# Performance work log

Hardware: AMD Instinct MI355X
Metric: run time of the kernel (lower is better)

The kernel has to match this reference:

```python
import jax, jax.numpy as jnp
import numpy as np

NUM_HEADS = 16
HEAD_DIM = 64
HIDDEN = NUM_HEADS * HEAD_DIM  # 1024
B, S = 2, 2048
INV_NORM = 1.0 / np.sqrt(HEAD_DIM)


def setup_inputs() -> dict:
    key = jax.random.key(0)
    ks = jax.random.split(key, 8)
    hidden_states = jax.random.normal(ks[0], (1, B, S, HIDDEN), dtype=jnp.float32)
    residual = jax.random.normal(ks[1], (B, S, HIDDEN), dtype=jnp.float32)
    # ALiBi bias per (batch*head) broadcast over query positions: [B*H, 1, S]
    slopes = 2.0 ** (-8.0 * (jnp.arange(1, NUM_HEADS + 1, dtype=jnp.float32) / NUM_HEADS))
    pos = jnp.arange(S, dtype=jnp.float32)
    alibi = (slopes[:, None] * pos[None, :])[None]  # [1, H, S]
    alibi = jnp.broadcast_to(alibi, (B, NUM_HEADS, S)).reshape(B * NUM_HEADS, 1, S)
    # causal mask: True = masked out
    attention_mask = jnp.triu(jnp.ones((S, S), dtype=jnp.bool_), k=1)[None, None]  # [1,1,S,S]
    attention_mask = jnp.broadcast_to(attention_mask, (B, 1, S, S))
    W_qkv = jax.random.normal(ks[2], (3 * HIDDEN, HIDDEN), dtype=jnp.float32) * 0.02
    b_qkv = jax.random.normal(ks[3], (3 * HIDDEN,), dtype=jnp.float32) * 0.02
    W_dense = jax.random.normal(ks[4], (HIDDEN, HIDDEN), dtype=jnp.float32) * 0.02
    b_dense = jax.random.normal(ks[5], (HIDDEN,), dtype=jnp.float32) * 0.02
    return {
        "hidden_states": hidden_states,
        "residual": residual,
        "alibi": alibi,
        "attention_mask": attention_mask,
        "W_qkv": W_qkv,
        "b_qkv": b_qkv,
        "W_dense": W_dense,
        "b_dense": b_dense,
    }


def reference(hidden_states, residual, alibi, attention_mask, W_qkv, b_qkv, W_dense, b_dense):
    x = hidden_states[0]  # [B, S, H]
    b, s, _ = x.shape
    fused = x @ W_qkv.T + b_qkv  # [B, S, 3H]
    # Bloom interleaved split: [B, S, nh, 3, hd]
    qkv = fused.reshape(b, s, NUM_HEADS, 3, HEAD_DIM)
    q = jnp.transpose(qkv[..., 0, :], (0, 2, 1, 3))  # [B, nh, S, hd]
    k = jnp.transpose(qkv[..., 1, :], (0, 2, 1, 3))
    v = jnp.transpose(qkv[..., 2, :], (0, 2, 1, 3))
    # baddbmm: alibi + inv_norm * q @ k^T
    scores = jnp.einsum("bhqd,bhkd->bhqk", q, k) * INV_NORM
    scores = scores + alibi.reshape(b, NUM_HEADS, 1, s)  # [B, nh, S, S]
    neg_min = jnp.finfo(scores.dtype).min
    scores = jnp.where(attention_mask, neg_min, scores)
    probs = jax.nn.softmax(scores.astype(jnp.float32), axis=-1).astype(x.dtype)
    ctx = jnp.einsum("bhqk,bhkd->bhqd", probs, v)  # [B, nh, S, hd]
    ctx = jnp.transpose(ctx, (0, 2, 1, 3)).reshape(b, s, HIDDEN)  # merge_heads
    out = ctx @ W_dense.T + b_dense
    return out + residual  # dropout_add, eval mode
```

## Files before the change

### kernel.cpp

```cpp
#include <hip/hip_runtime.h>
#include <hip/hip_bf16.h>

#define NUM_HEADS 16
#define HEAD_DIM  64
#define HIDDEN    1024
#define BATCH     2
#define SEQ       2048
#define K_DIM     1024
#define INV_NORM  0.125f
#define LOG2E     1.4426950408889634f
#define IN2       (INV_NORM * LOG2E)

typedef __attribute__((ext_vector_type(4)))  float f32x4;
typedef __attribute__((ext_vector_type(16))) float f32x16;
typedef __attribute__((ext_vector_type(8)))  short bf16x8;
typedef __attribute__((ext_vector_type(4)))  unsigned int u32x4;
typedef __attribute__((ext_vector_type(2)))  unsigned int u32x2;
typedef unsigned short u16;

__device__ inline u16 f2bf(float f) {
    __hip_bfloat16 h = __float2bfloat16(f);
    return __builtin_bit_cast(u16, h);
}
__device__ inline float bf2f(u16 u) {
    unsigned int v = ((unsigned int)u) << 16;
    return __builtin_bit_cast(float, v);
}
__device__ inline float fexp2(float x) { return __builtin_exp2f(x); }

__device__ inline f32x16 mfma32(bf16x8 a, bf16x8 b, f32x16 c) {
    return __builtin_amdgcn_mfma_f32_32x32x16_bf16(a, b, c, 0, 0, 0);
}

__device__ inline void gl_lds16(const u16* g, u16* s) {
    __builtin_amdgcn_global_load_lds(
        (const __attribute__((address_space(1))) unsigned int*)g,
        (__attribute__((address_space(3))) unsigned int*)s, 16, 0, 0);
}

__global__ __launch_bounds__(256) void cvt_all(
        const float* __restrict__ x, const float* __restrict__ wq,
        const float* __restrict__ wd,
        u16* __restrict__ xb, u16* __restrict__ wqb, u16* __restrict__ wdb) {
    int i = (blockIdx.x * 256 + threadIdx.x) * 4;
    const float* s; u16* d; int off;
    if (i < 4194304)      { s = x;  d = xb;  off = i; }
    else if (i < 7340032) { s = wq; d = wqb; off = i - 4194304; }
    else                  { s = wd; d = wdb; off = i - 7340032; }
    const float4 v = *reinterpret_cast<const float4*>(s + off);
    ushort4 o;
    o.x = f2bf(v.x); o.y = f2bf(v.y); o.z = f2bf(v.z); o.w = f2bf(v.w);
    *reinterpret_cast<ushort4*>(d + off) = o;
}

#define GEMM_CORE(A_, B_)                                                              \
    const int tid = threadIdx.x;                                                       \
    const int w = tid >> 6, l = tid & 63;                                              \
    const int la = l & 31, hi = l >> 5;                                                \
    const int wr = w >> 1, wc = w & 1;                                                 \
    const int kperm = (((l & 7) ^ (l >> 3)) << 3);                                     \
    const u16* gA = A_ + (size_t)(mblk + w * 32 + (l >> 3)) * K_DIM + kperm;           \
    const u16* gB = B_ + (size_t)(nblk + w * 32 + (l >> 3)) * K_DIM + kperm;           \
    const int sca = (la & 7) << 3;                                                     \
    f32x16 acc[2][2] = {};                                                             \
    for (int kt = 0; kt < 16; ++kt) {                                                  \
        const int ko = kt * 64;                                                        \
        _Pragma("unroll")                                                              \
        for (int i = 0; i < 4; ++i) {                                                  \
            gl_lds16(gA + i * 8 * K_DIM + ko, &As[(w * 32 + i * 8) * 64]);             \
            gl_lds16(gB + i * 8 * K_DIM + ko, &Bs[(w * 32 + i * 8) * 64]);             \
        }                                                                              \
        asm volatile("s_waitcnt vmcnt(0)" ::: "memory");                               \
        __syncthreads();                                                               \
        const u16* pA = &As[(wr * 64 + la) * 64];                                      \
        const u16* pB = &Bs[(wc * 64 + la) * 64];                                      \
        _Pragma("unroll")                                                              \
        for (int kk = 0; kk < 4; ++kk) {                                               \
            const int co = (kk * 16 + hi * 8) ^ sca;                                   \
            bf16x8 a0 = *reinterpret_cast<const bf16x8*>(pA + co);                     \
            bf16x8 a1 = *reinterpret_cast<const bf16x8*>(pA + 32 * 64 + co);           \
            bf16x8 b0 = *reinterpret_cast<const bf16x8*>(pB + co);                     \
            bf16x8 b1 = *reinterpret_cast<const bf16x8*>(pB + 32 * 64 + co);           \
            acc[0][0] = mfma32(a0, b0, acc[0][0]);                                     \
            acc[0][1] = mfma32(a0, b1, acc[0][1]);                                     \
            acc[1][0] = mfma32(a1, b0, acc[1][0]);                                     \
            acc[1][1] = mfma32(a1, b1, acc[1][1]);                                     \
        }                                                                              \
        __syncthreads();                                                               \
    }

__global__ __launch_bounds__(256) void gemm_qkv(
        const u16* __restrict__ A, const u16* __restrict__ W,
        const float* __restrict__ bias,
        u16* __restrict__ qo, u16* __restrict__ ko2, u16* __restrict__ vTo) {
    __shared__ u16 As[128 * 64];
    __shared__ u16 Bs[128 * 64];
    int lin = blockIdx.x;
    int g = lin & 7, i2 = lin >> 3;
    const int mblk = ((g & 3) * 8 + (i2 & 7)) * 128;
    const int nblk = ((g >> 2) * 12 + (i2 >> 3)) * 128;
    GEMM_CORE(A, W)
    #pragma unroll
    for (int mi = 0; mi < 2; ++mi)
    #pragma unroll
    for (int ni = 0; ni < 2; ++ni) {
        int c = nblk + wc * 64 + ni * 32 + la;
        int h = c / 192, rem = c - h * 192;
        int which = rem >> 6, d = rem & 63;
        float bv = bias[c];
        #pragma unroll
        for (int r = 0; r < 16; ++r) {
            int m = mblk + wr * 64 + mi * 32 + (r & 3) + 8 * (r >> 2) + 4 * hi;
            int bb = m >> 11, s = m & (SEQ - 1);
            int bh = bb * NUM_HEADS + h;
            int t = s >> 5;
            size_t tb = ((size_t)(bh * 64 + t)) * 2048;
            u16 o = f2bf(acc[mi][ni][r] + bv);
            if (which == 2) {
                int dblk = d >> 5, ra = d & 31;
                int k = s & 31, ks = k >> 4, hf = (k >> 3) & 1, e = k & 7;
                vTo[tb + (dblk * 2 + ks) * 512 + hf * 256 + ra * 8 + e] = o;
            } else {
                int kk = d >> 4, hf = (d >> 3) & 1, e = d & 7, ra = s & 31;
                size_t off = tb + kk * 512 + hf * 256 + ra * 8 + e;
                if (which == 0) qo[off] = o;
                else            ko2[off] = o;
            }
        }
    }
}

__global__ __launch_bounds__(256) void gemm_dense(
        const u16* __restrict__ A, const u16* __restrict__ W,
        const float* __restrict__ bias, const float* __restrict__ residual,
        float* __restrict__ out) {
    __shared__ u16 As[128 * 64];
    __shared__ u16 Bs[128 * 64];
    int lin = blockIdx.x;
    int g = lin & 7, i2 = lin >> 3;
    const int mblk = ((g & 1) * 16 + (i2 & 15)) * 128;
    const int nblk = ((g >> 1) * 2 + (i2 >> 4)) * 128;
    GEMM_CORE(A, W)
    #pragma unroll
    for (int mi = 0; mi < 2; ++mi)
    #pragma unroll
    for (int ni = 0; ni < 2; ++ni) {
        int c = nblk + wc * 64 + ni * 32 + la;
        float bv = bias[c];
        #pragma unroll
        for (int r = 0; r < 16; ++r) {
            int m = mblk + wr * 64 + mi * 32 + (r & 3) + 8 * (r >> 2) + 4 * hi;
            out[(size_t)m * HIDDEN + c] = acc[mi][ni][r] + bv + residual[(size_t)m * HIDDEN + c];
        }
    }
}

__global__ __launch_bounds__(256) void knorm_max(const u16* __restrict__ Kf,
                                                 float* __restrict__ kn,
                                                 unsigned int* __restrict__ ctr) {
    if (blockIdx.x == 0 && threadIdx.x < 8) ctr[threadIdx.x] = 0;
    __shared__ float red[256];
    const int bh = blockIdx.x;
    float mx = 0.f;
    for (int s = threadIdx.x; s < SEQ; s += 256) {
        const u16* kp = Kf + ((size_t)(bh * 64 + (s >> 5))) * 2048 + (s & 31) * 8;
        float ss = 0.f;
        #pragma unroll
        for (int kk = 0; kk < 4; ++kk)
        #pragma unroll
        for (int hf = 0; hf < 2; ++hf) {
            bf16x8 v = *reinterpret_cast<const bf16x8*>(kp + kk * 512 + hf * 256);
            #pragma unroll
            for (int e = 0; e < 8; ++e) {
                float f = bf2f((u16)v[e]);
                ss = fmaf(f, f, ss);
            }
        }
        mx = fmaxf(mx, ss);
    }
    red[threadIdx.x] = mx;
    __syncthreads();
    for (int off = 128; off; off >>= 1) {
        if (threadIdx.x < (unsigned)off)
            red[threadIdx.x] = fmaxf(red[threadIdx.x], red[threadIdx.x + off]);
        __syncthreads();
    }
    if (threadIdx.x == 0) kn[bh] = sqrtf(red[0]);
}


#define LOADT(P, tt) {                                                        \
    const u16* kp_ = kbase + (size_t)(tt) * 2048;                             \
    P##k0 = *reinterpret_cast<const bf16x8*>(kp_);                            \
    P##k1 = *reinterpret_cast<const bf16x8*>(kp_ + 512);                      \
    P##k2 = *reinterpret_cast<const bf16x8*>(kp_ + 1024);                     \
    P##k3 = *reinterpret_cast<const bf16x8*>(kp_ + 1536);                     \
    const u16* vp_ = vbase + (size_t)(tt) * 2048;                             \
    P##v0 = *reinterpret_cast<const bf16x8*>(vp_);                            \
    P##v1 = *reinterpret_cast<const bf16x8*>(vp_ + 512);                      \
    P##v2 = *reinterpret_cast<const bf16x8*>(vp_ + 1024);                     \
    P##v3 = *reinterpret_cast<const bf16x8*>(vp_ + 1536);                     \
}

#define STEP(P, N, tcur, tnxt, DIAG) {                                        \
    f32x16 sca_ = {}, scb_ = {};                                              \
    sca_ = mfma32(P##k0, qf0, sca_);                                          \
    scb_ = mfma32(P##k1, qf1, scb_);                                          \
    sca_ = mfma32(P##k2, qf2, sca_);                                          \
    scb_ = mfma32(P##k3, qf3, scb_);                                          \
    LOADT(N, tnxt)                                                            \
    const float Dt_ = slope2 * (float)((tcur) * 32 - qw);                     \
    float p[16];                                                              \
    _Pragma("unroll")                                                         \
    for (int r = 0; r < 16; ++r)                                              \
        p[r] = __builtin_amdgcn_exp2f(fmaf(sca_[r] + scb_[r], IN2, cl[r] + Dt_)); \
    if (DIAG) {                                                               \
        _Pragma("unroll")                                                     \
        for (int r = 0; r < 16; ++r) {                                        \
            int kr_ = (r & 3) + 8 * (r >> 2) + 4 * hi;                        \
            if (kr_ > la) p[r] = 0.f;                                         \
        }                                                                     \
    }                                                                         \
    l_i += ((p[0] + p[1]) + (p[2] + p[3])) + ((p[4] + p[5]) + (p[6] + p[7]))  \
         + ((p[8] + p[9]) + (p[10] + p[11])) + ((p[12] + p[13]) + (p[14] + p[15])); \
    unsigned pk_[8];                                                          \
    _Pragma("unroll")                                                         \
    for (int m = 0; m < 4; ++m) {                                             \
        unsigned b0_ = __builtin_bit_cast(unsigned, p[4 * m])     + 0x8000u;  \
        unsigned b1_ = __builtin_bit_cast(unsigned, p[4 * m + 1]) + 0x8000u;  \
        unsigned b2_ = __builtin_bit_cast(unsigned, p[4 * m + 2]) + 0x8000u;  \
        unsigned b3_ = __builtin_bit_cast(unsigned, p[4 * m + 3]) + 0x8000u;  \
        pk_[2 * m]     = __builtin_amdgcn_perm(b1_, b0_, 0x07060302u);        \
        pk_[2 * m + 1] = __builtin_amdgcn_perm(b3_, b2_, 0x07060302u);        \
    }                                                                         \
    u32x2 r0_ = __builtin_amdgcn_permlane32_swap(pk_[0], pk_[2], false, false); \
    u32x2 r1_ = __builtin_amdgcn_permlane32_swap(pk_[1], pk_[3], false, false); \
    u32x2 r2_ = __builtin_amdgcn_permlane32_swap(pk_[4], pk_[6], false, false); \
    u32x2 r3_ = __builtin_amdgcn_permlane32_swap(pk_[5], pk_[7], false, false); \
    u32x4 pb0_, pb1_;                                                         \
    pb0_[0] = r0_[0]; pb0_[1] = r1_[0]; pb0_[2] = r0_[1]; pb0_[3] = r1_[1];   \
    pb1_[0] = r2_[0]; pb1_[1] = r3_[0]; pb1_[2] = r2_[1]; pb1_[3] = r3_[1];   \
    bf16x8 pf0_ = __builtin_bit_cast(bf16x8, pb0_);                           \
    bf16x8 pf1_ = __builtin_bit_cast(bf16x8, pb1_);                           \
    o0 = mfma32(P##v0, pf0_, o0);                                             \
    o0 = mfma32(P##v1, pf1_, o0);                                             \
    o1 = mfma32(P##v2, pf0_, o1);                                             \
    o1 = mfma32(P##v3, pf1_, o1);                                             \
}

__global__ __launch_bounds__(256) void attn(
        const u16* __restrict__ Qf, const u16* __restrict__ Kf,
        const u16* __restrict__ Vf, const float* __restrict__ alibi,
        const float* __restrict__ kn, u16* __restrict__ ctx,
        unsigned int* __restrict__ ctr) {
    __shared__ float o_l[4][64][33];
    __shared__ float ml[4][32];
    __shared__ unsigned int s_idx;
    const int grp  = blockIdx.x & 7;
    const int wave = __builtin_amdgcn_readfirstlane(threadIdx.x >> 6);
    const int lane = threadIdx.x & 63;
    const int la = lane & 31, hi = lane >> 5;

    for (;;) {
        if (threadIdx.x == 0) s_idx = atomicAdd(ctr + grp, 1u);
        __syncthreads();
        const unsigned int idx = s_idx;
        if (idx >= 256) return;
        int h, b, qt;
        if (idx < 128) { h = 15 - grp; qt = 63 - (int)(idx >> 1); b = idx & 1; }
        else           { h = grp; int j = idx - 128; qt = 63 - (j >> 1); b = j & 1; }
        const int bh = b * 16 + h;
        const int qw = qt * 32;
        const size_t tbh = (size_t)bh * 64;
        const float slope2 = alibi[(size_t)bh * SEQ + 1] * LOG2E;

        const u16* qp = Qf + (tbh + qt) * 2048 + lane * 8;
        bf16x8 qf0 = *reinterpret_cast<const bf16x8*>(qp);
        bf16x8 qf1 = *reinterpret_cast<const bf16x8*>(qp + 512);
        bf16x8 qf2 = *reinterpret_cast<const bf16x8*>(qp + 1024);
        bf16x8 qf3 = *reinterpret_cast<const bf16x8*>(qp + 1536);

        float qss = 0.f;
        #pragma unroll
        for (int e = 0; e < 8; ++e) {
            float f;
            f = bf2f((u16)qf0[e]); qss = fmaf(f, f, qss);
            f = bf2f((u16)qf1[e]); qss = fmaf(f, f, qss);
            f = bf2f((u16)qf2[e]); qss = fmaf(f, f, qss);
            f = bf2f((u16)qf3[e]); qss = fmaf(f, f, qss);
        }
        qss += __shfl_xor(qss, 32);
        float qmx = qss;
        #pragma unroll
        for (int off = 1; off <= 16; off <<= 1) qmx = fmaxf(qmx, __shfl_xor(qmx, off));
        const float kb = sqrtf(qmx) * kn[bh] * IN2;

        const float Wf = (47.f + 2.f * kb) / slope2;
        const int lo_k = qw - 31 - (int)Wf;
        const int t_lo = lo_k <= 0 ? 0 : ((lo_k + 31) >> 5);

        float cl[16];
        #pragma unroll
        for (int r = 0; r < 16; ++r)
            cl[r] = slope2 * (float)((r & 3) + 8 * (r >> 2) + 4 * hi - la) - kb;

        f32x16 o0 = {}, o1 = {};
        float l_i = 0.f;

        const int t0 = qt - wave;
        if (t0 >= t_lo) {
            const u16* kbase = Kf + tbh * 2048 + lane * 8;
            const u16* vbase = Vf + tbh * 2048 + lane * 8;
            const int nit = ((t0 - t_lo) >> 2) + 1;
            bf16x8 ak0, ak1, ak2, ak3, av0, av1, av2, av3;
            bf16x8 bk0, bk1, bk2, bk3, bv0, bv1, bv2, bv3;
            LOADT(a, t0)
            {
                const int tn1 = (nit > 1) ? t0 - 4 : t0;
                if (wave == 0) { STEP(a, b, t0, tn1, 1) }
                else           { STEP(a, b, t0, tn1, 0) }
            }
            int i = 1;
            while (i < nit) {
                {
                    const int tc = t0 - 4 * i;
                    const int tn = (i + 1 < nit) ? tc - 4 : tc;
                    STEP(b, a, tc, tn, 0)
                }
                ++i;
                if (i >= nit) break;
                {
                    const int tc = t0 - 4 * i;
                    const int tn = (i + 1 < nit) ? tc - 4 : tc;
                    STEP(a, b, tc, tn, 0)
                }
                ++i;
            }
        }

        l_i += __shfl_xor(l_i, 32);
        if (hi == 0) ml[wave][la] = l_i;
        #pragma unroll
        for (int r = 0; r < 16; ++r) {
            int d = (r & 3) + 8 * (r >> 2) + 4 * hi;
            o_l[wave][d][la]      = o0[r];
            o_l[wave][d + 32][la] = o1[r];
        }
        __syncthreads();

        const int q  = threadIdx.x >> 3;
        const int d0 = (threadIdx.x & 7) * 8;
        float L = ml[0][q] + ml[1][q] + ml[2][q] + ml[3][q];
        float inv = 1.0f / L;
        unsigned int packed[4];
        #pragma unroll
        for (int e2 = 0; e2 < 4; ++e2) {
            float Oa = o_l[0][d0 + 2 * e2][q] + o_l[1][d0 + 2 * e2][q]
                     + o_l[2][d0 + 2 * e2][q] + o_l[3][d0 + 2 * e2][q];
            float Ob = o_l[0][d0 + 2 * e2 + 1][q] + o_l[1][d0 + 2 * e2 + 1][q]
                     + o_l[2][d0 + 2 * e2 + 1][q] + o_l[3][d0 + 2 * e2 + 1][q];
            packed[e2] = (unsigned)f2bf(Oa * inv) | ((unsigned)f2bf(Ob * inv) << 16);
        }
        const int bb = bh >> 4, hh = bh & 15;
        u32x4 pv; pv[0] = packed[0]; pv[1] = packed[1]; pv[2] = packed[2]; pv[3] = packed[3];
        *reinterpret_cast<u32x4*>(
            &ctx[((size_t)(bb * SEQ + qw + q)) * HIDDEN + hh * HEAD_DIM + d0]) = pv;
    }
}

extern "C" void kernel_launch(void* const* d_in, const int* in_sizes, int n_in,
                              void* d_out, int out_size, void* d_ws, size_t ws_size,
                              hipStream_t stream) {
    const float* x        = (const float*)d_in[0];
    const float* residual = (const float*)d_in[1];
    const float* alibi    = (const float*)d_in[2];
    const float* W_qkv    = (const float*)d_in[4];
    const float* b_qkv    = (const float*)d_in[5];
    const float* W_dense  = (const float*)d_in[6];
    const float* b_dense  = (const float*)d_in[7];
    float* out = (float*)d_out;

    char* ws = (char*)d_ws;
    u16* xb  = (u16*)(ws);
    u16* wqb = (u16*)(ws + 8388608);
    u16* wdb = (u16*)(ws + 14680064);
    u16* q   = (u16*)(ws + 16777216);
    u16* k   = (u16*)(ws + 25165824);
    u16* vT  = (u16*)(ws + 33554432);
    u16* ctx = (u16*)(ws + 41943040);
    float* kn = (float*)(ws + 50331648);
    unsigned int* ctr = (unsigned int*)(ws + 50331648 + 256);

    cvt_all<<<8192, 256, 0, stream>>>(x, W_qkv, W_dense, xb, wqb, wdb);
    gemm_qkv<<<768, 256, 0, stream>>>(xb, wqb, b_qkv, q, k, vT);
    knorm_max<<<32, 256, 0, stream>>>(k, kn, ctr);
    attn<<<1024, 256, 0, stream>>>(q, k, vT, alibi, kn, ctx, ctr);
    gemm_dense<<<256, 256, 0, stream>>>(ctx, wdb, b_dense, residual, out);
}
```

Measured before the change: 132.0 us.

## Double-buffer LDS tiles in shared GEMM core with smaller K step

The shared GEMM core for the QKV and dense projections now uses two LDS buffers with a K tile of 32 instead of one buffer with a K tile of 64. The next tile's global-to-LDS loads are issued before the MFMAs on the current tile, so load latency can overlap with compute. The XOR swizzle is adapted to the 32-wide rows. Total LDS per block stays the same, but there are twice as many iterations and barriers, and the wait for the next tile now sits at the end of each iteration.

```diff
diff --git a/kernel.cpp b/kernel.cpp
--- a/kernel.cpp
+++ b/kernel.cpp
@@ -26,7 +26,6 @@
     unsigned int v = ((unsigned int)u) << 16;
     return __builtin_bit_cast(float, v);
 }
-__device__ inline float fexp2(float x) { return __builtin_exp2f(x); }
 
 __device__ inline f32x16 mfma32(bf16x8 a, bf16x8 b, f32x16 c) {
     return __builtin_amdgcn_mfma_f32_32x32x16_bf16(a, b, c, 0, 0, 0);
@@ -58,43 +57,50 @@
     const int w = tid >> 6, l = tid & 63;                                              \
     const int la = l & 31, hi = l >> 5;                                                \
     const int wr = w >> 1, wc = w & 1;                                                 \
-    const int kperm = (((l & 7) ^ (l >> 3)) << 3);                                     \
-    const u16* gA = A_ + (size_t)(mblk + w * 32 + (l >> 3)) * K_DIM + kperm;           \
-    const u16* gB = B_ + (size_t)(nblk + w * 32 + (l >> 3)) * K_DIM + kperm;           \
-    const int sca = (la & 7) << 3;                                                     \
+    const int kperm = (((l & 3) ^ ((l >> 2) & 3)) << 3);                               \
+    const u16* gA = A_ + (size_t)(mblk + w * 32 + (l >> 2)) * K_DIM + kperm;           \
+    const u16* gB = B_ + (size_t)(nblk + w * 32 + (l >> 2)) * K_DIM + kperm;           \
     f32x16 acc[2][2] = {};                                                             \
-    for (int kt = 0; kt < 16; ++kt) {                                                  \
-        const int ko = kt * 64;                                                        \
+    gl_lds16(gA,               &As[0][(w * 32) * 32]);                                 \
+    gl_lds16(gA + 16 * K_DIM,  &As[0][(w * 32 + 16) * 32]);                            \
+    gl_lds16(gB,               &Bs[0][(w * 32) * 32]);                                 \
+    gl_lds16(gB + 16 * K_DIM,  &Bs[0][(w * 32 + 16) * 32]);                            \
+    asm volatile("s_waitcnt vmcnt(0)" ::: "memory");                                   \
+    __syncthreads();                                                                   \
+    int buf = 0;                                                                       \
+    for (int kt = 0; kt < 32; ++kt) {                                                  \
+        if (kt < 31) {                                                                 \
+            const int ko = (kt + 1) * 32;                                              \
+            gl_lds16(gA + ko,              &As[buf ^ 1][(w * 32) * 32]);               \
+            gl_lds16(gA + ko + 16 * K_DIM, &As[buf ^ 1][(w * 32 + 16) * 32]);          \
+            gl_lds16(gB + ko,              &Bs[buf ^ 1][(w * 32) * 32]);               \
+            gl_lds16(gB + ko + 16 * K_DIM, &Bs[buf ^ 1][(w * 32 + 16) * 32]);          \
+        }                                                                              \
+        const u16* pA = &As[buf][(wr * 64 + la) * 32];                                 \
+        const u16* pB = &Bs[buf][(wc * 64 + la) * 32];                                 \
         _Pragma("unroll")                                                              \
-        for (int i = 0; i < 4; ++i) {                                                  \
-            gl_lds16(gA + i * 8 * K_DIM + ko, &As[(w * 32 + i * 8) * 64]);             \
-            gl_lds16(gB + i * 8 * K_DIM + ko, &Bs[(w * 32 + i * 8) * 64]);             \
-        }                                                                              \
-        asm volatile("s_waitcnt vmcnt(0)" ::: "memory");                               \
-        __syncthreads();                                                               \
-        const u16* pA = &As[(wr * 64 + la) * 64];                                      \
-        const u16* pB = &Bs[(wc * 64 + la) * 64];                                      \
-        _Pragma("unroll")                                                              \
-        for (int kk = 0; kk < 4; ++kk) {                                               \
-            const int co = (kk * 16 + hi * 8) ^ sca;                                   \
+        for (int kk = 0; kk < 2; ++kk) {                                               \
+            const int co = (((kk * 2 + hi) ^ (la & 3)) << 3);                          \
             bf16x8 a0 = *reinterpret_cast<const bf16x8*>(pA + co);                     \
-            bf16x8 a1 = *reinterpret_cast<const bf16x8*>(pA + 32 * 64 + co);           \
+            bf16x8 a1 = *reinterpret_cast<const bf16x8*>(pA + 32 * 32 + co);           \
             bf16x8 b0 = *reinterpret_cast<const bf16x8*>(pB + co);                     \
-            bf16x8 b1 = *reinterpret_cast<const bf16x8*>(pB + 32 * 64 + co);           \
+            bf16x8 b1 = *reinterpret_cast<const bf16x8*>(pB + 32 * 32 + co);           \
             acc[0][0] = mfma32(a0, b0, acc[0][0]);                                     \
             acc[0][1] = mfma32(a0, b1, acc[0][1]);                                     \
             acc[1][0] = mfma32(a1, b0, acc[1][0]);                                     \
             acc[1][1] = mfma32(a1, b1, acc[1][1]);                                     \
         }                                                                              \
+        asm volatile("s_waitcnt vmcnt(0)" ::: "memory");                               \
         __syncthreads();                                                               \
+        buf ^= 1;                                                                      \
     }
 
 __global__ __launch_bounds__(256) void gemm_qkv(
         const u16* __restrict__ A, const u16* __restrict__ W,
         const float* __restrict__ bias,
         u16* __restrict__ qo, u16* __restrict__ ko2, u16* __restrict__ vTo) {
-    __shared__ u16 As[128 * 64];
-    __shared__ u16 Bs[128 * 64];
+    __shared__ u16 As[2][128 * 32];
+    __shared__ u16 Bs[2][128 * 32];
     int lin = blockIdx.x;
     int g = lin & 7, i2 = lin >> 3;
     const int mblk = ((g & 3) * 8 + (i2 & 7)) * 128;
@@ -134,8 +140,8 @@
         const u16* __restrict__ A, const u16* __restrict__ W,
         const float* __restrict__ bias, const float* __restrict__ residual,
         float* __restrict__ out) {
-    __shared__ u16 As[128 * 64];
-    __shared__ u16 Bs[128 * 64];
+    __shared__ u16 As[2][128 * 32];
+    __shared__ u16 Bs[2][128 * 32];
     int lin = blockIdx.x;
     int g = lin & 7, i2 = lin >> 3;
     const int mblk = ((g & 1) * 16 + (i2 & 15)) * 128;
@@ -187,7 +193,6 @@
     }
     if (threadIdx.x == 0) kn[bh] = sqrtf(red[0]);
 }
-
 
 #define LOADT(P, tt) {                                                        \
     const u16* kp_ = kbase + (size_t)(tt) * 2048;                             \
```

Result: slower. 147.7 us (+11.9%).
